# Kernel tuning notes

Hardware: AMD Instinct MI355X
Metric: run time of the kernel (lower is better)

## Reference

```python
import jax, jax.numpy as jnp
import numpy as np

N = 8192      # number of mentions
NC = 30       # SETTINGS.n_cands
D = 300       # SETTINGS.d
WIN = 100     # context window size
TOPK = 25     # min(SETTINGS.attention_token_count, window_size)
NEG = -1e10   # mask fill value from original code


def setup_inputs() -> dict:
    key = jax.random.key(0)
    k1, k2, k3 = jax.random.split(key, 3)
    embeddings = jax.random.normal(k1, (N, NC, D), dtype=jnp.float32)
    tokenEmbeddings = jax.random.normal(k2, (N, WIN, D), dtype=jnp.float32)
    # ragged-style mask: first `len` tokens valid per mention
    lengths = jax.random.randint(k3, (N,), 1, WIN + 1)
    tokenMaskss = jnp.arange(WIN)[None, :] < lengths[:, None]
    B_diag1 = jnp.ones((D,), dtype=jnp.float32)
    B_diag2 = jnp.ones((D,), dtype=jnp.float32)
    return {
        "embeddings": embeddings,
        "tokenEmbeddings": tokenEmbeddings,
        "tokenMaskss": tokenMaskss,
        "B_diag1": B_diag1,
        "B_diag2": B_diag2,
    }


def reference(embeddings, tokenEmbeddings, tokenMaskss, B_diag1, B_diag2):
    # --- f_c: context embedding ---
    # diag_embed + matmul in torch == elementwise scale of token feature dim
    scores = jnp.einsum('ncd,nwd->ncw', embeddings, tokenEmbeddings * B_diag2)
    scores = jnp.where(tokenMaskss[:, None, :], scores, NEG)
    token_scores = jnp.max(scores, axis=1)
    best_scores, best_idx = jax.lax.top_k(token_scores, TOPK)   # (n, TOPK)
    best_tokens = jnp.take_along_axis(
        tokenEmbeddings, best_idx[:, :, None], axis=1)          # (n, TOPK, d)
    token_probs = jax.nn.softmax(best_scores, axis=1)
    # original renormalizes again (no-op numerically, kept for faithfulness)
    token_probs = token_probs / jnp.sum(token_probs, axis=1, keepdims=True)
    fcs = jnp.einsum('ntd,nt->nd', best_tokens, token_probs)    # (n, d)
    # --- psiss: diag-scaled dot with each candidate ---
    vals = jnp.einsum('ncd,nd->nc', embeddings, fcs * B_diag1)  # (n, n_cands)
    return vals
```

## Files before the change

kernel.cpp:

```cpp
#include <hip/hip_runtime.h>
#include <math.h>

#define NC    30
#define D     300
#define WIN   100
#define TOPK  25
#define NEGV  -1e10f
#define NKS   19
#define AST   312

typedef __attribute__((ext_vector_type(8)))  short short8;
typedef __attribute__((ext_vector_type(16))) float f32x16;
typedef __attribute__((ext_vector_type(4)))  unsigned int uint4v;

__device__ inline unsigned short bftrunc(float f) {
    return (unsigned short)(__builtin_bit_cast(unsigned int, f) >> 16);
}
__device__ inline float bfval(unsigned short b) {
    return __builtin_bit_cast(float, (unsigned int)b << 16);
}
__device__ inline void split8(const float* v, short8& hi, short8& lo) {
    #pragma unroll
    for (int j = 0; j < 8; ++j) {
        unsigned short hb = bftrunc(v[j]);
        float lf = v[j] - bfval(hb);
        hi[j] = (short)hb;
        lo[j] = (short)bftrunc(lf);
    }
}

__global__ __launch_bounds__(256, 4)
void fused_mention_kernel(const float* __restrict__ E,
                          const float* __restrict__ T,
                          const void*  __restrict__ maskp,
                          const float* __restrict__ B1,
                          const float* __restrict__ B2,
                          float* __restrict__ out)
{
    const int n     = blockIdx.x;
    const int tid   = threadIdx.x;
    const int wv    = tid >> 6;
    const int lane  = tid & 63;
    const int arow  = lane & 31;
    const int khalf = (lane >> 5) * 8;

    __shared__ __align__(16) short Ah[NC * AST];
    __shared__ __align__(16) short Al[NC * AST];
    __shared__ __align__(16) float fcsL[D];
    __shared__ float ts[WIN];
    __shared__ float bscore[TOPK];
    __shared__ int   bidx[TOPK];
    __shared__ float bprob[TOPK];
    __shared__ float vredS[4][32];

    if (tid < WIN) ts[tid] = NEGV;

    int found;
    {
        const uint4v* m4 = (const uint4v*)maskp;
        uint4v w = m4[wv * 64 + lane];
        found = (((w.x | w.y | w.z | w.w) & 0xFFFFFF00u) != 0u) ? 1 : 0;
    }
    const bool bytemask = (__ballot(found) != 0ULL);

    int v0m = 0, v1m = 0;
    if (bytemask) {
        const unsigned char* mb = (const unsigned char*)maskp + (size_t)n * WIN;
        v0m = mb[lane] != 0;
        if (lane + 64 < WIN) v1m = mb[lane + 64] != 0;
    } else {
        const int* mi = (const int*)maskp + (size_t)n * WIN;
        v0m = mi[lane] != 0;
        if (lane + 64 < WIN) v1m = mi[lane + 64] != 0;
    }
    const int L  = __popcll(__ballot(v0m)) + __popcll(__ballot(v1m));
    const int Lc = (L > 0) ? L : 1;

    int neq = 0;
    #pragma unroll
    for (int k = 0; k < 5; ++k) {
        const int d = lane + 64 * k;
        if (d < D) neq |= (B1[d] != B2[d]) ? 1 : 0;
    }
    const bool beq = (__ballot(neq) == 0ULL);

    {
        const int srow = tid & 31;
        const int scol = tid >> 5;
        if (srow < NC) {
            #pragma unroll
            for (int k = 0; k < 5; ++k) {
                const int c8 = scol + 8 * k;
                if (c8 < 38) {
                    const int col = c8 * 8;
                    const float* src = E + ((size_t)n * NC + srow) * D + col;
                    float v[8];
                    float4 q0 = *reinterpret_cast<const float4*>(src);
                    float4 b0 = *reinterpret_cast<const float4*>(B2 + col);
                    v[0] = q0.x * b0.x; v[1] = q0.y * b0.y;
                    v[2] = q0.z * b0.z; v[3] = q0.w * b0.w;
                    if (c8 < 37) {
                        float4 q1 = *reinterpret_cast<const float4*>(src + 4);
                        float4 b1 = *reinterpret_cast<const float4*>(B2 + col + 4);
                        v[4] = q1.x * b1.x; v[5] = q1.y * b1.y;
                        v[6] = q1.z * b1.z; v[7] = q1.w * b1.w;
                    } else {
                        v[4] = v[5] = v[6] = v[7] = 0.f;
                    }
                    short8 hi, lo;
                    split8(v, hi, lo);
                    *reinterpret_cast<short8*>(Ah + srow * AST + col) = hi;
                    *reinterpret_cast<short8*>(Al + srow * AST + col) = lo;
                }
            }
        }
    }

    const int ntiles = (L + 31) >> 5;
    const float* Tn = T + (size_t)n * WIN * D;
    const float* bp = Tn + (size_t)min(wv * 32 + arow, Lc - 1) * D;

    float4 q0r[4], q1r[4];
    if (wv < ntiles) {
        #pragma unroll
        for (int s = 0; s < 4; ++s) {
            const int kb = 16 * s + khalf;
            q0r[s] = *reinterpret_cast<const float4*>(bp + kb);
            q1r[s] = *reinterpret_cast<const float4*>(bp + kb + 4);
        }
    }
    __syncthreads();

    f32x16 c;
    #pragma unroll
    for (int r = 0; r < 16; ++r) c[r] = 0.f;
    if (wv < ntiles) {
        const int t0 = wv * 32;
        const int aoff = min(arow, NC - 1) * AST + khalf;
        #pragma unroll
        for (int s = 0; s < NKS; ++s) {
            const int slot = s & 3;
            float4 q0 = q0r[slot], q1 = q1r[slot];
            if (s + 4 < NKS) {
                const int kb2 = 16 * (s + 4) + khalf;
                q0r[slot] = *reinterpret_cast<const float4*>(bp + kb2);
                q1r[slot] = (kb2 + 8 <= D)
                          ? *reinterpret_cast<const float4*>(bp + kb2 + 4)
                          : make_float4(0.f, 0.f, 0.f, 0.f);
            }
            short8 ah = *reinterpret_cast<const short8*>(Ah + aoff + 16 * s);
            short8 al = *reinterpret_cast<const short8*>(Al + aoff + 16 * s);
            float v[8] = {q0.x, q0.y, q0.z, q0.w, q1.x, q1.y, q1.z, q1.w};
            short8 bh, bl;
            split8(v, bh, bl);
            c = __builtin_amdgcn_mfma_f32_32x32x16_bf16(ah, bh, c, 0, 0, 0);
            c = __builtin_amdgcn_mfma_f32_32x32x16_bf16(al, bh, c, 0, 0, 0);
            c = __builtin_amdgcn_mfma_f32_32x32x16_bf16(ah, bl, c, 0, 0, 0);
        }
        if (lane >= 32) { c[14] = -__builtin_inff(); c[15] = -__builtin_inff(); }
        float m = c[0];
        #pragma unroll
        for (int r = 1; r < 16; ++r) m = fmaxf(m, c[r]);
        m = fmaxf(m, __shfl_xor(m, 32));
        if (lane < 32 && t0 + arow < L) ts[t0 + arow] = m;
    }
    __syncthreads();

    if (tid < 64) {
        float va = ts[tid];
        float vb = (tid + 64 < WIN) ? ts[tid + 64] : -__builtin_inff();
        float mx = 0.f;
        for (int t = 0; t < TOPK; ++t) {
            float v0; int i0;
            if (vb > va) { v0 = vb; i0 = tid + 64; } else { v0 = va; i0 = tid; }
            #pragma unroll
            for (int s = 32; s >= 1; s >>= 1) {
                float ov = __shfl_xor(v0, s);
                int   oi = __shfl_xor(i0, s);
                if (ov > v0 || (ov == v0 && oi < i0)) { v0 = ov; i0 = oi; }
            }
            if (t == 0) mx = v0;
            if (tid == 0) { bscore[t] = v0; bidx[t] = i0; }
            if (i0 == tid) va = -__builtin_inff();
            else if (i0 == tid + 64) vb = -__builtin_inff();
        }
        float sc = (tid < TOPK) ? bscore[tid] : 0.f;
        float p  = (tid < TOPK) ? expf(sc - mx) : 0.f;
        float s1 = p;
        #pragma unroll
        for (int s = 32; s >= 1; s >>= 1) s1 += __shfl_xor(s1, s);
        p = p / s1;
        float s2 = p;
        #pragma unroll
        for (int s = 32; s >= 1; s >>= 1) s2 += __shfl_xor(s2, s);
        p = p / s2;
        if (tid < TOPK) bprob[tid] = p;
    }
    __syncthreads();

    if (beq) {
        float vacc[16];
        #pragma unroll
        for (int r = 0; r < 16; ++r) vacc[r] = 0.f;
        if (wv < ntiles) {
            for (int t = 0; t < TOPK; ++t) {
                const int ix = bidx[t];
                if ((ix >> 5) == wv) {
                    const float p = bprob[t];
                    if ((lane & 31) == (ix & 31)) {
                        #pragma unroll
                        for (int r = 0; r < 16; ++r) vacc[r] += p * c[r];
                    }
                }
            }
        }
        #pragma unroll
        for (int r = 0; r < 16; ++r) {
            float s = vacc[r];
            s += __shfl_xor(s, 1);  s += __shfl_xor(s, 2);
            s += __shfl_xor(s, 4);  s += __shfl_xor(s, 8);
            s += __shfl_xor(s, 16);
            vacc[r] = s;
        }
        if ((lane & 31) == 0) {
            #pragma unroll
            for (int r = 0; r < 16; ++r) {
                const int row = (r & 3) + 8 * (r >> 2) + 4 * (lane >> 5);
                vredS[wv][row] = vacc[r];
            }
        }
        __syncthreads();
        if (tid < NC) {
            out[(size_t)n * NC + tid] = vredS[0][tid] + vredS[1][tid]
                                      + vredS[2][tid] + vredS[3][tid];
        }
    } else {
        for (int d = tid; d < D; d += 256) {
            float acc = 0.f;
            #pragma unroll 5
            for (int t = 0; t < TOPK; ++t)
                acc += bprob[t] * Tn[(size_t)bidx[t] * D + d];
            fcsL[d] = acc;
        }
        __syncthreads();
        {
            const int dg = tid >> 5;
            const int d0 = dg * 40;
            const bool full = (dg < 7);
            const int cg = arow;
            const bool cok = (cg < NC);
            float acc2 = 0.f;
            const float* Erow = E + ((size_t)n * NC + (cok ? cg : 0)) * D + d0;
            #pragma unroll
            for (int j = 0; j < 5; ++j) {
                float4 ev = *reinterpret_cast<const float4*>(Erow + 4 * j);
                float4 bv = *reinterpret_cast<const float4*>(B1 + d0 + 4 * j);
                float4 fv = *reinterpret_cast<const float4*>(fcsL + d0 + 4 * j);
                acc2 += ev.x * bv.x * fv.x + ev.y * bv.y * fv.y
                      + ev.z * bv.z * fv.z + ev.w * bv.w * fv.w;
            }
            if (full) {
                #pragma unroll
                for (int j = 5; j < 10; ++j) {
                    float4 ev = *reinterpret_cast<const float4*>(Erow + 4 * j);
                    float4 bv = *reinterpret_cast<const float4*>(B1 + d0 + 4 * j);
                    float4 fv = *reinterpret_cast<const float4*>(fcsL + d0 + 4 * j);
                    acc2 += ev.x * bv.x * fv.x + ev.y * bv.y * fv.y
                          + ev.z * bv.z * fv.z + ev.w * bv.w * fv.w;
                }
            }
            if (!cok) acc2 = 0.f;
            acc2 += __shfl_xor(acc2, 32);
            if (lane < 32) vredS[wv][cg] = acc2;
        }
        __syncthreads();
        if (tid < NC) {
            out[(size_t)n * NC + tid] = vredS[0][tid] + vredS[1][tid]
                                      + vredS[2][tid] + vredS[3][tid];
        }
    }
}

extern "C" void kernel_launch(void* const* d_in, const int* in_sizes, int n_in,
                              void* d_out, int out_size, void* d_ws, size_t ws_size,
                              hipStream_t stream)
{
    const float* E  = (const float*)d_in[0];
    const float* T  = (const float*)d_in[1];
    const void*  M  = d_in[2];
    const float* B1 = (const float*)d_in[3];
    const float* B2 = (const float*)d_in[4];
    float* out = (float*)d_out;
    const int n = in_sizes[0] / (NC * D);
    fused_mention_kernel<<<n, 256, 0, stream>>>(E, T, M, B1, B2, out);
}
```

Measured before the change: 278.1 us.

## Load candidate embeddings directly into registers and compute top-k redundantly per wave

```diff
diff --git a/kernel.cpp b/kernel.cpp
--- a/kernel.cpp
+++ b/kernel.cpp
@@ -7,7 +7,6 @@
 #define TOPK  25
 #define NEGV  -1e10f
 #define NKS   19
-#define AST   312
 
 typedef __attribute__((ext_vector_type(8)))  short short8;
 typedef __attribute__((ext_vector_type(16))) float f32x16;
@@ -44,16 +43,11 @@
     const int arow  = lane & 31;
     const int khalf = (lane >> 5) * 8;
 
-    __shared__ __align__(16) short Ah[NC * AST];
-    __shared__ __align__(16) short Al[NC * AST];
+    __shared__ float ts[WIN];
     __shared__ __align__(16) float fcsL[D];
-    __shared__ float ts[WIN];
-    __shared__ float bscore[TOPK];
-    __shared__ int   bidx[TOPK];
-    __shared__ float bprob[TOPK];
+    __shared__ int   bidxL[TOPK];
+    __shared__ float bprobL[TOPK];
     __shared__ float vredS[4][32];
-
-    if (tid < WIN) ts[tid] = NEGV;
 
     int found;
     {
@@ -84,59 +78,29 @@
     }
     const bool beq = (__ballot(neq) == 0ULL);
 
-    {
-        const int srow = tid & 31;
-        const int scol = tid >> 5;
-        if (srow < NC) {
-            #pragma unroll
-            for (int k = 0; k < 5; ++k) {
-                const int c8 = scol + 8 * k;
-                if (c8 < 38) {
-                    const int col = c8 * 8;
-                    const float* src = E + ((size_t)n * NC + srow) * D + col;
-                    float v[8];
-                    float4 q0 = *reinterpret_cast<const float4*>(src);
-                    float4 b0 = *reinterpret_cast<const float4*>(B2 + col);
-                    v[0] = q0.x * b0.x; v[1] = q0.y * b0.y;
-                    v[2] = q0.z * b0.z; v[3] = q0.w * b0.w;
-                    if (c8 < 37) {
-                        float4 q1 = *reinterpret_cast<const float4*>(src + 4);
-                        float4 b1 = *reinterpret_cast<const float4*>(B2 + col + 4);
-                        v[4] = q1.x * b1.x; v[5] = q1.y * b1.y;
-                        v[6] = q1.z * b1.z; v[7] = q1.w * b1.w;
-                    } else {
-                        v[4] = v[5] = v[6] = v[7] = 0.f;
-                    }
-                    short8 hi, lo;
-                    split8(v, hi, lo);
-                    *reinterpret_cast<short8*>(Ah + srow * AST + col) = hi;
-                    *reinterpret_cast<short8*>(Al + srow * AST + col) = lo;
-                }
-            }
-        }
-    }
-
     const int ntiles = (L + 31) >> 5;
+    const int t0 = wv * 32;
     const float* Tn = T + (size_t)n * WIN * D;
-    const float* bp = Tn + (size_t)min(wv * 32 + arow, Lc - 1) * D;
-
-    float4 q0r[4], q1r[4];
+    const float* bp = Tn + (size_t)min(t0 + arow, Lc - 1) * D;
+    const float* ep = E + ((size_t)n * NC + min(arow, NC - 1)) * D;
+
+    f32x16 c;
+    #pragma unroll
+    for (int r = 0; r < 16; ++r) c[r] = 0.f;
+    float m = NEGV;
+
     if (wv < ntiles) {
+        f32x16 cB;
+        #pragma unroll
+        for (int r = 0; r < 16; ++r) cB[r] = 0.f;
+
+        float4 q0r[4], q1r[4];
         #pragma unroll
         for (int s = 0; s < 4; ++s) {
             const int kb = 16 * s + khalf;
             q0r[s] = *reinterpret_cast<const float4*>(bp + kb);
             q1r[s] = *reinterpret_cast<const float4*>(bp + kb + 4);
         }
-    }
-    __syncthreads();
-
-    f32x16 c;
-    #pragma unroll
-    for (int r = 0; r < 16; ++r) c[r] = 0.f;
-    if (wv < ntiles) {
-        const int t0 = wv * 32;
-        const int aoff = min(arow, NC - 1) * AST + khalf;
         #pragma unroll
         for (int s = 0; s < NKS; ++s) {
             const int slot = s & 3;
@@ -148,55 +112,75 @@
                           ? *reinterpret_cast<const float4*>(bp + kb2 + 4)
                           : make_float4(0.f, 0.f, 0.f, 0.f);
             }
-            short8 ah = *reinterpret_cast<const short8*>(Ah + aoff + 16 * s);
-            short8 al = *reinterpret_cast<const short8*>(Al + aoff + 16 * s);
+            const int kb = 16 * s + khalf;
+            float av[8] = {0.f, 0.f, 0.f, 0.f, 0.f, 0.f, 0.f, 0.f};
+            {
+                float4 e0 = *reinterpret_cast<const float4*>(ep + kb);
+                float4 g0 = *reinterpret_cast<const float4*>(B2 + kb);
+                av[0] = e0.x * g0.x; av[1] = e0.y * g0.y;
+                av[2] = e0.z * g0.z; av[3] = e0.w * g0.w;
+                if (kb + 8 <= D) {
+                    float4 e1 = *reinterpret_cast<const float4*>(ep + kb + 4);
+                    float4 g1 = *reinterpret_cast<const float4*>(B2 + kb + 4);
+                    av[4] = e1.x * g1.x; av[5] = e1.y * g1.y;
+                    av[6] = e1.z * g1.z; av[7] = e1.w * g1.w;
+                }
+            }
+            short8 ah, al;
+            split8(av, ah, al);
             float v[8] = {q0.x, q0.y, q0.z, q0.w, q1.x, q1.y, q1.z, q1.w};
             short8 bh, bl;
             split8(v, bh, bl);
-            c = __builtin_amdgcn_mfma_f32_32x32x16_bf16(ah, bh, c, 0, 0, 0);
-            c = __builtin_amdgcn_mfma_f32_32x32x16_bf16(al, bh, c, 0, 0, 0);
-            c = __builtin_amdgcn_mfma_f32_32x32x16_bf16(ah, bl, c, 0, 0, 0);
-        }
+            if (s & 1) {
+                cB = __builtin_amdgcn_mfma_f32_32x32x16_bf16(ah, bh, cB, 0, 0, 0);
+                cB = __builtin_amdgcn_mfma_f32_32x32x16_bf16(al, bh, cB, 0, 0, 0);
+                cB = __builtin_amdgcn_mfma_f32_32x32x16_bf16(ah, bl, cB, 0, 0, 0);
+            } else {
+                c  = __builtin_amdgcn_mfma_f32_32x32x16_bf16(ah, bh, c, 0, 0, 0);
+                c  = __builtin_amdgcn_mfma_f32_32x32x16_bf16(al, bh, c, 0, 0, 0);
+                c  = __builtin_amdgcn_mfma_f32_32x32x16_bf16(ah, bl, c, 0, 0, 0);
+            }
+        }
+        #pragma unroll
+        for (int r = 0; r < 16; ++r) c[r] += cB[r];
         if (lane >= 32) { c[14] = -__builtin_inff(); c[15] = -__builtin_inff(); }
-        float m = c[0];
+        m = c[0];
         #pragma unroll
         for (int r = 1; r < 16; ++r) m = fmaxf(m, c[r]);
         m = fmaxf(m, __shfl_xor(m, 32));
-        if (lane < 32 && t0 + arow < L) ts[t0 + arow] = m;
-    }
+    }
+    if (lane < 32 && t0 + arow < WIN)
+        ts[t0 + arow] = (wv < ntiles && t0 + arow < L) ? m : NEGV;
     __syncthreads();
 
-    if (tid < 64) {
-        float va = ts[tid];
-        float vb = (tid + 64 < WIN) ? ts[tid + 64] : -__builtin_inff();
-        float mx = 0.f;
-        for (int t = 0; t < TOPK; ++t) {
-            float v0; int i0;
-            if (vb > va) { v0 = vb; i0 = tid + 64; } else { v0 = va; i0 = tid; }
-            #pragma unroll
-            for (int s = 32; s >= 1; s >>= 1) {
-                float ov = __shfl_xor(v0, s);
-                int   oi = __shfl_xor(i0, s);
-                if (ov > v0 || (ov == v0 && oi < i0)) { v0 = ov; i0 = oi; }
-            }
-            if (t == 0) mx = v0;
-            if (tid == 0) { bscore[t] = v0; bidx[t] = i0; }
-            if (i0 == tid) va = -__builtin_inff();
-            else if (i0 == tid + 64) vb = -__builtin_inff();
-        }
-        float sc = (tid < TOPK) ? bscore[tid] : 0.f;
-        float p  = (tid < TOPK) ? expf(sc - mx) : 0.f;
-        float s1 = p;
-        #pragma unroll
-        for (int s = 32; s >= 1; s >>= 1) s1 += __shfl_xor(s1, s);
-        p = p / s1;
-        float s2 = p;
-        #pragma unroll
-        for (int s = 32; s >= 1; s >>= 1) s2 += __shfl_xor(s2, s);
-        p = p / s2;
-        if (tid < TOPK) bprob[tid] = p;
-    }
-    __syncthreads();
+    const float NINF = -__builtin_inff();
+    float va = ts[lane];
+    float vb = (lane + 64 < WIN) ? ts[lane + 64] : NINF;
+    float sc = 0.f, mx = 0.f;
+    int   ixr = 0;
+    for (int t = 0; t < TOPK; ++t) {
+        float v0; int i0;
+        if (vb > va) { v0 = vb; i0 = lane + 64; } else { v0 = va; i0 = lane; }
+        #pragma unroll
+        for (int s = 32; s >= 1; s >>= 1) {
+            float ov = __shfl_xor(v0, s);
+            int   oi = __shfl_xor(i0, s);
+            if (ov > v0 || (ov == v0 && oi < i0)) { v0 = ov; i0 = oi; }
+        }
+        if (t == 0) mx = v0;
+        if (lane == t) { sc = v0; ixr = i0; }
+        if (i0 == lane) va = NINF;
+        else if (i0 == lane + 64) vb = NINF;
+    }
+    float p = (lane < TOPK) ? expf(sc - mx) : 0.f;
+    float s1 = p;
+    #pragma unroll
+    for (int s = 32; s >= 1; s >>= 1) s1 += __shfl_xor(s1, s);
+    p = p / s1;
+    float s2 = p;
+    #pragma unroll
+    for (int s = 32; s >= 1; s >>= 1) s2 += __shfl_xor(s2, s);
+    p = p / s2;
 
     if (beq) {
         float vacc[16];
@@ -204,12 +188,12 @@
         for (int r = 0; r < 16; ++r) vacc[r] = 0.f;
         if (wv < ntiles) {
             for (int t = 0; t < TOPK; ++t) {
-                const int ix = bidx[t];
-                if ((ix >> 5) == wv) {
-                    const float p = bprob[t];
-                    if ((lane & 31) == (ix & 31)) {
+                const float pb = __shfl(p, t);
+                const int   ib = __shfl(ixr, t);
+                if ((ib >> 5) == wv) {
+                    if ((lane & 31) == (ib & 31)) {
                         #pragma unroll
-                        for (int r = 0; r < 16; ++r) vacc[r] += p * c[r];
+                        for (int r = 0; r < 16; ++r) vacc[r] += pb * c[r];
                     }
                 }
             }
@@ -230,16 +214,17 @@
             }
         }
         __syncthreads();
-        if (tid < NC) {
+        if (tid < NC)
             out[(size_t)n * NC + tid] = vredS[0][tid] + vredS[1][tid]
                                       + vredS[2][tid] + vredS[3][tid];
-        }
     } else {
+        if (wv == 0 && lane < TOPK) { bprobL[lane] = p; bidxL[lane] = ixr; }
+        __syncthreads();
         for (int d = tid; d < D; d += 256) {
             float acc = 0.f;
             #pragma unroll 5
             for (int t = 0; t < TOPK; ++t)
-                acc += bprob[t] * Tn[(size_t)bidx[t] * D + d];
+                acc += bprobL[t] * Tn[(size_t)bidxL[t] * D + d];
             fcsL[d] = acc;
         }
         __syncthreads();
@@ -274,10 +259,9 @@
             if (lane < 32) vredS[wv][cg] = acc2;
         }
         __syncthreads();
-        if (tid < NC) {
+        if (tid < NC)
             out[(size_t)n * NC + tid] = vredS[0][tid] + vredS[1][tid]
                                       + vredS[2][tid] + vredS[3][tid];
-        }
     }
 }
 
```

Result: slower. 290.8 us (+4.6%).

## Score tokens with single-pass bf16 MFMA, recompute only top-k tokens precisely in one wave

Applied to the files above, without the earlier changes.

```diff
diff --git a/kernel.cpp b/kernel.cpp
--- a/kernel.cpp
+++ b/kernel.cpp
@@ -46,14 +46,7 @@
 
     __shared__ __align__(16) short Ah[NC * AST];
     __shared__ __align__(16) short Al[NC * AST];
-    __shared__ __align__(16) float fcsL[D];
     __shared__ float ts[WIN];
-    __shared__ float bscore[TOPK];
-    __shared__ int   bidx[TOPK];
-    __shared__ float bprob[TOPK];
-    __shared__ float vredS[4][32];
-
-    if (tid < WIN) ts[tid] = NEGV;
 
     int found;
     {
@@ -117,8 +110,10 @@
     }
 
     const int ntiles = (L + 31) >> 5;
+    const int t0 = wv * 32;
     const float* Tn = T + (size_t)n * WIN * D;
-    const float* bp = Tn + (size_t)min(wv * 32 + arow, Lc - 1) * D;
+    const float* bp = Tn + (size_t)min(t0 + arow, Lc - 1) * D;
+    const int aoff = min(arow, NC - 1) * AST + khalf;
 
     float4 q0r[4], q1r[4];
     if (wv < ntiles) {
@@ -131,12 +126,11 @@
     }
     __syncthreads();
 
-    f32x16 c;
-    #pragma unroll
-    for (int r = 0; r < 16; ++r) c[r] = 0.f;
+    float m = NEGV;
     if (wv < ntiles) {
-        const int t0 = wv * 32;
-        const int aoff = min(arow, NC - 1) * AST + khalf;
+        f32x16 c;
+        #pragma unroll
+        for (int r = 0; r < 16; ++r) c[r] = 0.f;
         #pragma unroll
         for (int s = 0; s < NKS; ++s) {
             const int slot = s & 3;
@@ -149,74 +143,111 @@
                           : make_float4(0.f, 0.f, 0.f, 0.f);
             }
             short8 ah = *reinterpret_cast<const short8*>(Ah + aoff + 16 * s);
+            short8 bh;
+            bh[0] = (short)bftrunc(q0.x); bh[1] = (short)bftrunc(q0.y);
+            bh[2] = (short)bftrunc(q0.z); bh[3] = (short)bftrunc(q0.w);
+            bh[4] = (short)bftrunc(q1.x); bh[5] = (short)bftrunc(q1.y);
+            bh[6] = (short)bftrunc(q1.z); bh[7] = (short)bftrunc(q1.w);
+            c = __builtin_amdgcn_mfma_f32_32x32x16_bf16(ah, bh, c, 0, 0, 0);
+        }
+        if (lane >= 32) { c[14] = -__builtin_inff(); c[15] = -__builtin_inff(); }
+        m = c[0];
+        #pragma unroll
+        for (int r = 1; r < 16; ++r) m = fmaxf(m, c[r]);
+        m = fmaxf(m, __shfl_xor(m, 32));
+    }
+    if (lane < 32 && t0 + arow < WIN)
+        ts[t0 + arow] = (wv < ntiles && t0 + arow < L) ? m : NEGV;
+    __syncthreads();
+
+    if (wv != 0) return;
+
+    const float NINF = -__builtin_inff();
+    float va = ts[lane];
+    float vb = (lane + 64 < WIN) ? ts[lane + 64] : NINF;
+    int ixr = 0;
+    for (int t = 0; t < TOPK; ++t) {
+        float v0; int i0;
+        if (vb > va) { v0 = vb; i0 = lane + 64; } else { v0 = va; i0 = lane; }
+        #pragma unroll
+        for (int s = 32; s >= 1; s >>= 1) {
+            float ov = __shfl_xor(v0, s);
+            int   oi = __shfl_xor(i0, s);
+            if (ov > v0 || (ov == v0 && oi < i0)) { v0 = ov; i0 = oi; }
+        }
+        if (lane == t) ixr = i0;
+        if (i0 == lane) va = NINF;
+        else if (i0 == lane + 64) vb = NINF;
+    }
+    const int bidx_col = __shfl(ixr, min(arow, TOPK - 1));
+    const bool colok = (arow < TOPK) && (bidx_col < L);
+
+    const float* wp = Tn + (size_t)bidx_col * D;
+    f32x16 c;  f32x16 cB;
+    #pragma unroll
+    for (int r = 0; r < 16; ++r) { c[r] = 0.f; cB[r] = 0.f; }
+    {
+        float4 e0r[4], e1r[4];
+        #pragma unroll
+        for (int s = 0; s < 4; ++s) {
+            const int kb = 16 * s + khalf;
+            e0r[s] = *reinterpret_cast<const float4*>(wp + kb);
+            e1r[s] = *reinterpret_cast<const float4*>(wp + kb + 4);
+        }
+        #pragma unroll
+        for (int s = 0; s < NKS; ++s) {
+            const int slot = s & 3;
+            float4 q0 = e0r[slot], q1 = e1r[slot];
+            if (s + 4 < NKS) {
+                const int kb2 = 16 * (s + 4) + khalf;
+                e0r[slot] = *reinterpret_cast<const float4*>(wp + kb2);
+                e1r[slot] = (kb2 + 8 <= D)
+                          ? *reinterpret_cast<const float4*>(wp + kb2 + 4)
+                          : make_float4(0.f, 0.f, 0.f, 0.f);
+            }
+            short8 ah = *reinterpret_cast<const short8*>(Ah + aoff + 16 * s);
             short8 al = *reinterpret_cast<const short8*>(Al + aoff + 16 * s);
             float v[8] = {q0.x, q0.y, q0.z, q0.w, q1.x, q1.y, q1.z, q1.w};
             short8 bh, bl;
             split8(v, bh, bl);
-            c = __builtin_amdgcn_mfma_f32_32x32x16_bf16(ah, bh, c, 0, 0, 0);
-            c = __builtin_amdgcn_mfma_f32_32x32x16_bf16(al, bh, c, 0, 0, 0);
-            c = __builtin_amdgcn_mfma_f32_32x32x16_bf16(ah, bl, c, 0, 0, 0);
-        }
-        if (lane >= 32) { c[14] = -__builtin_inff(); c[15] = -__builtin_inff(); }
-        float m = c[0];
-        #pragma unroll
-        for (int r = 1; r < 16; ++r) m = fmaxf(m, c[r]);
-        m = fmaxf(m, __shfl_xor(m, 32));
-        if (lane < 32 && t0 + arow < L) ts[t0 + arow] = m;
-    }
-    __syncthreads();
-
-    if (tid < 64) {
-        float va = ts[tid];
-        float vb = (tid + 64 < WIN) ? ts[tid + 64] : -__builtin_inff();
-        float mx = 0.f;
-        for (int t = 0; t < TOPK; ++t) {
-            float v0; int i0;
-            if (vb > va) { v0 = vb; i0 = tid + 64; } else { v0 = va; i0 = tid; }
-            #pragma unroll
-            for (int s = 32; s >= 1; s >>= 1) {
-                float ov = __shfl_xor(v0, s);
-                int   oi = __shfl_xor(i0, s);
-                if (ov > v0 || (ov == v0 && oi < i0)) { v0 = ov; i0 = oi; }
-            }
-            if (t == 0) mx = v0;
-            if (tid == 0) { bscore[t] = v0; bidx[t] = i0; }
-            if (i0 == tid) va = -__builtin_inff();
-            else if (i0 == tid + 64) vb = -__builtin_inff();
-        }
-        float sc = (tid < TOPK) ? bscore[tid] : 0.f;
-        float p  = (tid < TOPK) ? expf(sc - mx) : 0.f;
-        float s1 = p;
-        #pragma unroll
-        for (int s = 32; s >= 1; s >>= 1) s1 += __shfl_xor(s1, s);
-        p = p / s1;
-        float s2 = p;
-        #pragma unroll
-        for (int s = 32; s >= 1; s >>= 1) s2 += __shfl_xor(s2, s);
-        p = p / s2;
-        if (tid < TOPK) bprob[tid] = p;
-    }
-    __syncthreads();
+            if (s & 1) {
+                cB = __builtin_amdgcn_mfma_f32_32x32x16_bf16(ah, bh, cB, 0, 0, 0);
+                cB = __builtin_amdgcn_mfma_f32_32x32x16_bf16(al, bh, cB, 0, 0, 0);
+                cB = __builtin_amdgcn_mfma_f32_32x32x16_bf16(ah, bl, cB, 0, 0, 0);
+            } else {
+                c  = __builtin_amdgcn_mfma_f32_32x32x16_bf16(ah, bh, c, 0, 0, 0);
+                c  = __builtin_amdgcn_mfma_f32_32x32x16_bf16(al, bh, c, 0, 0, 0);
+                c  = __builtin_amdgcn_mfma_f32_32x32x16_bf16(ah, bl, c, 0, 0, 0);
+            }
+        }
+        #pragma unroll
+        for (int r = 0; r < 16; ++r) c[r] += cB[r];
+    }
+    if (lane >= 32) { c[14] = NINF; c[15] = NINF; }
+    float mt = c[0];
+    #pragma unroll
+    for (int r = 1; r < 16; ++r) mt = fmaxf(mt, c[r]);
+    mt = fmaxf(mt, __shfl_xor(mt, 32));
+    mt = colok ? mt : NEGV;
+
+    float mx = mt;
+    #pragma unroll
+    for (int s = 16; s >= 1; s >>= 1) mx = fmaxf(mx, __shfl_xor(mx, s));
+    float p = (arow < TOPK) ? expf(mt - mx) : 0.f;
+    float s1 = p;
+    #pragma unroll
+    for (int s = 16; s >= 1; s >>= 1) s1 += __shfl_xor(s1, s);
+    p = p / s1;
+    float s2 = p;
+    #pragma unroll
+    for (int s = 16; s >= 1; s >>= 1) s2 += __shfl_xor(s2, s);
+    p = p / s2;
 
     if (beq) {
         float vacc[16];
         #pragma unroll
-        for (int r = 0; r < 16; ++r) vacc[r] = 0.f;
-        if (wv < ntiles) {
-            for (int t = 0; t < TOPK; ++t) {
-                const int ix = bidx[t];
-                if ((ix >> 5) == wv) {
-                    const float p = bprob[t];
-                    if ((lane & 31) == (ix & 31)) {
-                        #pragma unroll
-                        for (int r = 0; r < 16; ++r) vacc[r] += p * c[r];
-                    }
-                }
-            }
-        }
-        #pragma unroll
         for (int r = 0; r < 16; ++r) {
-            float s = vacc[r];
+            float s = p * c[r];
             s += __shfl_xor(s, 1);  s += __shfl_xor(s, 2);
             s += __shfl_xor(s, 4);  s += __shfl_xor(s, 8);
             s += __shfl_xor(s, 16);
@@ -226,57 +257,40 @@
             #pragma unroll
             for (int r = 0; r < 16; ++r) {
                 const int row = (r & 3) + 8 * (r >> 2) + 4 * (lane >> 5);
-                vredS[wv][row] = vacc[r];
-            }
-        }
-        __syncthreads();
-        if (tid < NC) {
-            out[(size_t)n * NC + tid] = vredS[0][tid] + vredS[1][tid]
-                                      + vredS[2][tid] + vredS[3][tid];
+                if (row < NC) out[(size_t)n * NC + row] = vacc[r];
+            }
         }
     } else {
-        for (int d = tid; d < D; d += 256) {
-            float acc = 0.f;
-            #pragma unroll 5
-            for (int t = 0; t < TOPK; ++t)
-                acc += bprob[t] * Tn[(size_t)bidx[t] * D + d];
-            fcsL[d] = acc;
-        }
-        __syncthreads();
-        {
-            const int dg = tid >> 5;
-            const int d0 = dg * 40;
-            const bool full = (dg < 7);
-            const int cg = arow;
-            const bool cok = (cg < NC);
-            float acc2 = 0.f;
-            const float* Erow = E + ((size_t)n * NC + (cok ? cg : 0)) * D + d0;
-            #pragma unroll
-            for (int j = 0; j < 5; ++j) {
-                float4 ev = *reinterpret_cast<const float4*>(Erow + 4 * j);
-                float4 bv = *reinterpret_cast<const float4*>(B1 + d0 + 4 * j);
-                float4 fv = *reinterpret_cast<const float4*>(fcsL + d0 + 4 * j);
-                acc2 += ev.x * bv.x * fv.x + ev.y * bv.y * fv.y
-                      + ev.z * bv.z * fv.z + ev.w * bv.w * fv.w;
-            }
-            if (full) {
-                #pragma unroll
-                for (int j = 5; j < 10; ++j) {
-                    float4 ev = *reinterpret_cast<const float4*>(Erow + 4 * j);
-                    float4 bv = *reinterpret_cast<const float4*>(B1 + d0 + 4 * j);
-                    float4 fv = *reinterpret_cast<const float4*>(fcsL + d0 + 4 * j);
-                    acc2 += ev.x * bv.x * fv.x + ev.y * bv.y * fv.y
-                          + ev.z * bv.z * fv.z + ev.w * bv.w * fv.w;
-                }
-            }
-            if (!cok) acc2 = 0.f;
-            acc2 += __shfl_xor(acc2, 32);
-            if (lane < 32) vredS[wv][cg] = acc2;
-        }
-        __syncthreads();
-        if (tid < NC) {
-            out[(size_t)n * NC + tid] = vredS[0][tid] + vredS[1][tid]
-                                      + vredS[2][tid] + vredS[3][tid];
+        float fc[5] = {0.f, 0.f, 0.f, 0.f, 0.f};
+        for (int t = 0; t < TOPK; ++t) {
+            const float pb = __shfl(p, t);
+            const int   ib = __shfl(bidx_col, t);
+            const float* Trow = Tn + (size_t)ib * D;
+            #pragma unroll
+            for (int c5 = 0; c5 < 5; ++c5) {
+                const int dim = c5 * 64 + lane;
+                if (dim < D) fc[c5] += pb * Trow[dim];
+            }
+        }
+        float acc2[NC];
+        #pragma unroll
+        for (int cc = 0; cc < NC; ++cc) acc2[cc] = 0.f;
+        #pragma unroll
+        for (int c5 = 0; c5 < 5; ++c5) {
+            const int dim  = c5 * 64 + lane;
+            const int dimc = min(dim, D - 1);
+            const float g  = (dim < D) ? B1[dim] * fc[c5] : 0.f;
+            const float* Eb = E + (size_t)n * NC * D + dimc;
+            #pragma unroll
+            for (int cc = 0; cc < NC; ++cc)
+                acc2[cc] += Eb[(size_t)cc * D] * g;
+        }
+        #pragma unroll
+        for (int cc = 0; cc < NC; ++cc) {
+            float s = acc2[cc];
+            #pragma unroll
+            for (int sft = 32; sft >= 1; sft >>= 1) s += __shfl_xor(s, sft);
+            if (lane == cc) out[(size_t)n * NC + cc] = s;
         }
     }
 }
```

After: 342.7 us. +23.2%, slower.
